# Optimization experiments

Hardware: AMD Instinct MI355X
Metric: run time of the kernel (lower is better)

## Reference

```python
import jax, jax.numpy as jnp
import numpy as np

N_NODES = 100000
N_EDGES = 1600000
DIM = 128


def setup_inputs() -> dict:
    key = jax.random.key(0)
    k1, k2, k3, k4 = jax.random.split(key, 4)
    x = jax.random.normal(k1, (N_NODES, DIM), dtype=jnp.float32)
    edge_index = jax.random.randint(k2, (2, N_EDGES), 0, N_NODES, dtype=jnp.int64)
    scale = 1.0 / np.sqrt(DIM)
    W1 = jax.random.normal(k3, (DIM, DIM), dtype=jnp.float32) * scale
    W2 = jax.random.normal(k4, (DIM, DIM), dtype=jnp.float32) * scale
    b1 = jnp.zeros((DIM,), dtype=jnp.float32)
    b2 = jnp.zeros((DIM,), dtype=jnp.float32)
    return {"x": x, "edge_index": edge_index, "W1": W1, "b1": b1, "W2": W2, "b2": b2}


def _gcn_conv(x, src, dst, dinv, W, b, n):
    # linear transform first (PyG GCNConv), then normalized scatter-add aggregation
    h = x @ W                                   # [N, out]
    norm = dinv[src] * dinv[dst]                # [E+N]
    msg = h[src] * norm[:, None]                # [E+N, out]
    agg = jax.ops.segment_sum(msg, dst, num_segments=n)
    return agg + b


def reference(x, edge_index, W1, b1, W2, b2):
    n = x.shape[0]
    loops = jnp.arange(n, dtype=edge_index.dtype)
    src = jnp.concatenate([edge_index[0], loops])  # add self-loops
    dst = jnp.concatenate([edge_index[1], loops])
    deg = jax.ops.segment_sum(jnp.ones_like(src, dtype=x.dtype), dst, num_segments=n)
    dinv = jnp.where(deg > 0, jax.lax.rsqrt(deg), 0.0)  # D^{-1/2}
    h = _gcn_conv(x, src, dst, dinv, W1, b1, n)
    h = jax.nn.relu(h)
    out = _gcn_conv(h, src, dst, dinv, W2, b2, n)
    return out
```

## Files before the change

kernel.cpp:

```cpp
#include <hip/hip_runtime.h>
#include <hip/hip_bf16.h>
#include <hip/hip_fp16.h>

#define NN 100000
#define DIM 128
#define NB 391
#define BCAP 5120
#define SCAN_NB 391
#define GTILES ((NN + 63) / 64)

typedef _Float16 f16x8 __attribute__((ext_vector_type(8)));
typedef float f32x4 __attribute__((ext_vector_type(4)));

__global__ void k_zero(int* __restrict__ p, int n) {
    int i = blockIdx.x * blockDim.x + threadIdx.x;
    if (i < n) p[i] = 0;
}

__global__ void k_binA(const int* __restrict__ src, const int* __restrict__ dst,
                       int* __restrict__ bcur, int* __restrict__ binbuf, int E) {
    __shared__ int hist[NB];
    __shared__ int base[NB];
    const int t = threadIdx.x;
    for (int b = t; b < NB; b += 256) hist[b] = 0;
    __syncthreads();

    const int e0 = blockIdx.x * 4096;
    int mys[16], myd[16];
#pragma unroll
    for (int i = 0; i < 16; ++i) {
        const int e = e0 + i * 256 + t;
        int d = -1, s = 0;
        if (e < E) {
            d = dst[e];
            s = src[e];
            atomicAdd(&hist[d >> 8], 1);
        }
        mys[i] = s;
        myd[i] = d;
    }
    __syncthreads();

    for (int b = t; b < NB; b += 256) {
        const int h = hist[b];
        base[b] = h ? atomicAdd(&bcur[b], h) : 0;
    }
    __syncthreads();
    for (int b = t; b < NB; b += 256) hist[b] = 0;
    __syncthreads();

#pragma unroll
    for (int i = 0; i < 16; ++i) {
        const int d = myd[i];
        if (d >= 0) {
            const int b = d >> 8;
            const int loc = atomicAdd(&hist[b], 1);
            const int p = base[b] + loc;
            if (p < BCAP) binbuf[b * BCAP + p] = mys[i] | ((d & 255) << 17);
        }
    }
}

__global__ void k_binCount(const int* __restrict__ bcur, const int* __restrict__ binbuf,
                           int* __restrict__ degi) {
    __shared__ int cnt[256];
    const int b = blockIdx.x;
    const int t = threadIdx.x;
    cnt[t] = 0;
    __syncthreads();
    const int n = min(bcur[b], BCAP);
    const int* p = &binbuf[b * BCAP];
    for (int i = t; i < n; i += 256) atomicAdd(&cnt[p[i] >> 17], 1);
    __syncthreads();
    const int node = b * 256 + t;
    if (node < NN) degi[node] = cnt[t];
}

__global__ void k_scan1(const int* __restrict__ deg, int* __restrict__ bsum, int n) {
    __shared__ int red[256];
    const int t = threadIdx.x;
    const int i = blockIdx.x * 256 + t;
    red[t] = (i < n) ? deg[i] : 0;
    __syncthreads();
    for (int d = 128; d > 0; d >>= 1) {
        if (t < d) red[t] += red[t + d];
        __syncthreads();
    }
    if (t == 0) bsum[blockIdx.x] = red[0];
}

__global__ void k_scan2(int* __restrict__ bsum, int nb) {
    __shared__ int s[1024];
    const int t = threadIdx.x;
    const int v = (t < nb) ? bsum[t] : 0;
    s[t] = v;
    __syncthreads();
    int acc = v;
    for (int d = 1; d < 1024; d <<= 1) {
        const int o = (t >= d) ? s[t - d] : 0;
        __syncthreads();
        acc += o;
        s[t] = acc;
        __syncthreads();
    }
    if (t < nb) bsum[t] = acc - v;
}

__global__ void k_scan3d(const int* __restrict__ deg, const int* __restrict__ bsum,
                         int* __restrict__ rowptr, float* __restrict__ dinv, int n) {
    __shared__ int s[256];
    const int t = threadIdx.x;
    const int i = blockIdx.x * 256 + t;
    const int v = (i < n) ? deg[i] : 0;
    s[t] = v;
    __syncthreads();
    int acc = v;
    for (int d = 1; d < 256; d <<= 1) {
        const int o = (t >= d) ? s[t - d] : 0;
        __syncthreads();
        acc += o;
        s[t] = acc;
        __syncthreads();
    }
    const int ex = acc - v + bsum[blockIdx.x];
    if (i < n) {
        rowptr[i] = ex;
        dinv[i] = rsqrtf((float)(v + 1));
        if (i == n - 1) rowptr[n] = ex + v;
    }
}

template <int IN_HALF, int FILL>
__global__ void k_gemm(const float* __restrict__ inF, const _Float16* __restrict__ inH,
                       const float* __restrict__ W, const float* __restrict__ dinv,
                       const float* __restrict__ bin, _Float16* __restrict__ outH,
                       const int* __restrict__ rowptr, const int* __restrict__ bcur,
                       const int* __restrict__ binbuf, int* __restrict__ csr) {
    __shared__ int cur[256];
    const int t = threadIdx.x;

    if (FILL && blockIdx.x < NB) {
        const int b = blockIdx.x;
        const int node = b * 256 + t;
        cur[t] = (node < NN) ? rowptr[node] : 0;
        __syncthreads();
        const int n = min(bcur[b], BCAP);
        const int* p = &binbuf[b * BCAP];
        for (int i = t; i < n; i += 256) {
            const int v = p[i];
            const int pos = atomicAdd(&cur[v >> 17], 1);
            csr[pos] = v & 0x1FFFF;
        }
        return;
    }

    const int tile = blockIdx.x - (FILL ? NB : 0);
    const int row0 = tile * 64;
    const int wv   = t >> 6;
    const int l    = t & 63;
    const int l15  = l & 15;
    const int lk8  = (l >> 4) << 3;
    const int colw = wv << 5;

    f16x8 bf[2][4];
#pragma unroll
    for (int ct = 0; ct < 2; ++ct) {
#pragma unroll
        for (int kt = 0; kt < 4; ++kt) {
            const int n  = colw + ct * 16 + l15;
            const int k0 = kt * 32 + lk8;
            f16x8 v;
#pragma unroll
            for (int j = 0; j < 8; ++j) v[j] = (_Float16)W[(k0 + j) * DIM + n];
            bf[ct][kt] = v;
        }
    }

    f32x4 acc[4][2];
#pragma unroll
    for (int rt = 0; rt < 4; ++rt)
#pragma unroll
        for (int ct = 0; ct < 2; ++ct) acc[rt][ct] = (f32x4){0.f, 0.f, 0.f, 0.f};

#pragma unroll
    for (int rt = 0; rt < 4; ++rt) {
        int row = row0 + rt * 16 + l15;
        row = min(row, NN - 1);
        f16x8 a[4];
#pragma unroll
        for (int kt = 0; kt < 4; ++kt) {
            const int k0 = kt * 32 + lk8;
            if constexpr (IN_HALF) {
                const f16x8 h = *(const f16x8*)&inH[row * DIM + k0];
                const float dr = dinv[row];
                const float4 bb0 = *(const float4*)&bin[k0];
                const float4 bb1 = *(const float4*)&bin[k0 + 4];
                f16x8 v;
                v[0] = (_Float16)fmaxf(fmaf(dr, (float)h[0], bb0.x), 0.f);
                v[1] = (_Float16)fmaxf(fmaf(dr, (float)h[1], bb0.y), 0.f);
                v[2] = (_Float16)fmaxf(fmaf(dr, (float)h[2], bb0.z), 0.f);
                v[3] = (_Float16)fmaxf(fmaf(dr, (float)h[3], bb0.w), 0.f);
                v[4] = (_Float16)fmaxf(fmaf(dr, (float)h[4], bb1.x), 0.f);
                v[5] = (_Float16)fmaxf(fmaf(dr, (float)h[5], bb1.y), 0.f);
                v[6] = (_Float16)fmaxf(fmaf(dr, (float)h[6], bb1.z), 0.f);
                v[7] = (_Float16)fmaxf(fmaf(dr, (float)h[7], bb1.w), 0.f);
                a[kt] = v;
            } else {
                const float4 v0 = *(const float4*)&inF[row * DIM + k0];
                const float4 v1 = *(const float4*)&inF[row * DIM + k0 + 4];
                f16x8 v;
                v[0] = (_Float16)v0.x; v[1] = (_Float16)v0.y;
                v[2] = (_Float16)v0.z; v[3] = (_Float16)v0.w;
                v[4] = (_Float16)v1.x; v[5] = (_Float16)v1.y;
                v[6] = (_Float16)v1.z; v[7] = (_Float16)v1.w;
                a[kt] = v;
            }
        }
#pragma unroll
        for (int ct = 0; ct < 2; ++ct)
#pragma unroll
            for (int kt = 0; kt < 4; ++kt)
                acc[rt][ct] = __builtin_amdgcn_mfma_f32_16x16x32_f16(a[kt], bf[ct][kt],
                                                                    acc[rt][ct], 0, 0, 0);
    }

#pragma unroll
    for (int rt = 0; rt < 4; ++rt) {
#pragma unroll
        for (int r = 0; r < 4; ++r) {
            const int row = row0 + rt * 16 + ((l >> 4) << 2) + r;
            if (row < NN) {
                const float d = dinv[row];
                outH[row * DIM + colw + l15]      = (_Float16)(acc[rt][0][r] * d);
                outH[row * DIM + colw + 16 + l15] = (_Float16)(acc[rt][1][r] * d);
            }
        }
    }
}

template <int FINAL>
__global__ void k_gather(const __half* __restrict__ hs, __half* __restrict__ outH,
                         float* __restrict__ outF, const int* __restrict__ csr,
                         const int* __restrict__ rowptr, const float* __restrict__ dinv,
                         const float* __restrict__ b2) {
    const int w = (blockIdx.x * blockDim.x + threadIdx.x) >> 6;
    if (w >= NN) return;
    const int lane = threadIdx.x & 63;
    const int off  = lane << 1;

    const int start = __builtin_amdgcn_readfirstlane(rowptr[w]);
    const int end   = __builtin_amdgcn_readfirstlane(rowptr[w + 1]);

    float2 a0 = __half22float2(*(const __half2*)&hs[w * DIM + off]);
    float2 a1 = {0.f, 0.f}, a2 = {0.f, 0.f}, a3 = {0.f, 0.f};

    int j = start;
    for (; j + 3 < end; j += 4) {
        const int s0 = __builtin_amdgcn_readfirstlane(csr[j]);
        const int s1 = __builtin_amdgcn_readfirstlane(csr[j + 1]);
        const int s2 = __builtin_amdgcn_readfirstlane(csr[j + 2]);
        const int s3 = __builtin_amdgcn_readfirstlane(csr[j + 3]);
        const float2 v0 = __half22float2(*(const __half2*)&hs[s0 * DIM + off]);
        const float2 v1 = __half22float2(*(const __half2*)&hs[s1 * DIM + off]);
        const float2 v2 = __half22float2(*(const __half2*)&hs[s2 * DIM + off]);
        const float2 v3 = __half22float2(*(const __half2*)&hs[s3 * DIM + off]);
        a0.x += v0.x; a0.y += v0.y;
        a1.x += v1.x; a1.y += v1.y;
        a2.x += v2.x; a2.y += v2.y;
        a3.x += v3.x; a3.y += v3.y;
    }
    for (; j < end; ++j) {
        const int s0 = __builtin_amdgcn_readfirstlane(csr[j]);
        const float2 v0 = __half22float2(*(const __half2*)&hs[s0 * DIM + off]);
        a0.x += v0.x; a0.y += v0.y;
    }

    float2 r = {a0.x + a1.x + a2.x + a3.x, a0.y + a1.y + a2.y + a3.y};
    if constexpr (FINAL) {
        const float d = dinv[w];
        const float2 b = *(const float2*)&b2[off];
        r.x = fmaf(d, r.x, b.x);
        r.y = fmaf(d, r.y, b.y);
        *(float2*)&outF[w * DIM + off] = r;
    } else {
        *(__half2*)&outH[w * DIM + off] = __floats2half2_rn(r.x, r.y);
    }
}

extern "C" void kernel_launch(void* const* d_in, const int* in_sizes, int n_in,
                              void* d_out, int out_size, void* d_ws, size_t ws_size,
                              hipStream_t stream) {
    const float* x  = (const float*)d_in[0];
    const int*   ei = (const int*)d_in[1];
    const float* W1 = (const float*)d_in[2];
    const float* b1 = (const float*)d_in[3];
    const float* W2 = (const float*)d_in[4];
    const float* b2 = (const float*)d_in[5];
    float* out = (float*)d_out;

    const int E = in_sizes[1] / 2;
    const int* src = ei;
    const int* dst = ei + E;

    char* ws = (char*)d_ws;
    float*    dinv   = (float*)(ws);
    int*      degi   = (int*)  (ws + (1  << 20));
    int*      rowptr = (int*)  (ws + (2  << 20));
    int*      bsum   = (int*)  (ws + (3  << 20));
    int*      bcur   = (int*)  (ws + (3  << 20) + 65536);
    int*      csr    = (int*)  (ws + (4  << 20));
    int*      binbuf = (int*)  (ws + (11 << 20));
    _Float16* hs     = (_Float16*)(ws + (20 << 20));
    _Float16* agg1   = (_Float16*)(ws + (47 << 20));

    const int ABLK = (E + 4095) / 4096;

    k_zero    <<<(NB + 255) / 256, 256, 0, stream>>>(bcur, NB);
    k_binA    <<<ABLK, 256, 0, stream>>>(src, dst, bcur, binbuf, E);
    k_binCount<<<NB, 256, 0, stream>>>(bcur, binbuf, degi);
    k_scan1   <<<SCAN_NB, 256, 0, stream>>>(degi, bsum, NN);
    k_scan2   <<<1, 1024, 0, stream>>>(bsum, SCAN_NB);
    k_scan3d  <<<SCAN_NB, 256, 0, stream>>>(degi, bsum, rowptr, dinv, NN);

    k_gemm<0, 1><<<NB + GTILES, 256, 0, stream>>>(x, nullptr, W1, dinv, nullptr, hs,
                                                  rowptr, bcur, binbuf, csr);
    k_gather<0> <<<(NN * 64) / 256, 256, 0, stream>>>((const __half*)hs, (__half*)agg1,
                                                      nullptr, csr, rowptr, dinv, nullptr);

    k_gemm<1, 0><<<GTILES, 256, 0, stream>>>(nullptr, agg1, W2, dinv, b1, hs,
                                             rowptr, bcur, binbuf, csr);
    k_gather<1> <<<(NN * 64) / 256, 256, 0, stream>>>((const __half*)hs, nullptr, out,
                                                      csr, rowptr, dinv, b2);
}
```

Before: 236.7 us.

## Fuse first-layer gather into second GEMM and fold scan stages into neighbours

```diff
diff --git a/kernel.cpp b/kernel.cpp
--- a/kernel.cpp
+++ b/kernel.cpp
@@ -6,7 +6,6 @@
 #define DIM 128
 #define NB 391
 #define BCAP 5120
-#define SCAN_NB 391
 #define GTILES ((NN + 63) / 64)
 
 typedef _Float16 f16x8 __attribute__((ext_vector_type(8)));
@@ -62,8 +61,10 @@
 }
 
 __global__ void k_binCount(const int* __restrict__ bcur, const int* __restrict__ binbuf,
-                           int* __restrict__ degi) {
+                           int* __restrict__ degi, float* __restrict__ dinv,
+                           int* __restrict__ bsum) {
     __shared__ int cnt[256];
+    __shared__ int red[256];
     const int b = blockIdx.x;
     const int t = threadIdx.x;
     cnt[t] = 0;
@@ -73,20 +74,18 @@
     for (int i = t; i < n; i += 256) atomicAdd(&cnt[p[i] >> 17], 1);
     __syncthreads();
     const int node = b * 256 + t;
-    if (node < NN) degi[node] = cnt[t];
-}
-
-__global__ void k_scan1(const int* __restrict__ deg, int* __restrict__ bsum, int n) {
-    __shared__ int red[256];
-    const int t = threadIdx.x;
-    const int i = blockIdx.x * 256 + t;
-    red[t] = (i < n) ? deg[i] : 0;
+    const int c = cnt[t];
+    if (node < NN) {
+        degi[node] = c;
+        dinv[node] = rsqrtf((float)(c + 1));
+    }
+    red[t] = (node < NN) ? c : 0;
     __syncthreads();
     for (int d = 128; d > 0; d >>= 1) {
         if (t < d) red[t] += red[t + d];
         __syncthreads();
     }
-    if (t == 0) bsum[blockIdx.x] = red[0];
+    if (t == 0) bsum[b] = red[0];
 }
 
 __global__ void k_scan2(int* __restrict__ bsum, int nb) {
@@ -106,43 +105,35 @@
     if (t < nb) bsum[t] = acc - v;
 }
 
-__global__ void k_scan3d(const int* __restrict__ deg, const int* __restrict__ bsum,
-                         int* __restrict__ rowptr, float* __restrict__ dinv, int n) {
+__global__ void k_gemm1(const float* __restrict__ inF, const float* __restrict__ W,
+                        const float* __restrict__ dinv, _Float16* __restrict__ outH,
+                        const int* __restrict__ degi, const int* __restrict__ bsum,
+                        int* __restrict__ rowptr, const int* __restrict__ bcur,
+                        const int* __restrict__ binbuf, int* __restrict__ csr) {
     __shared__ int s[256];
-    const int t = threadIdx.x;
-    const int i = blockIdx.x * 256 + t;
-    const int v = (i < n) ? deg[i] : 0;
-    s[t] = v;
-    __syncthreads();
-    int acc = v;
-    for (int d = 1; d < 256; d <<= 1) {
-        const int o = (t >= d) ? s[t - d] : 0;
-        __syncthreads();
-        acc += o;
-        s[t] = acc;
-        __syncthreads();
-    }
-    const int ex = acc - v + bsum[blockIdx.x];
-    if (i < n) {
-        rowptr[i] = ex;
-        dinv[i] = rsqrtf((float)(v + 1));
-        if (i == n - 1) rowptr[n] = ex + v;
-    }
-}
-
-template <int IN_HALF, int FILL>
-__global__ void k_gemm(const float* __restrict__ inF, const _Float16* __restrict__ inH,
-                       const float* __restrict__ W, const float* __restrict__ dinv,
-                       const float* __restrict__ bin, _Float16* __restrict__ outH,
-                       const int* __restrict__ rowptr, const int* __restrict__ bcur,
-                       const int* __restrict__ binbuf, int* __restrict__ csr) {
     __shared__ int cur[256];
     const int t = threadIdx.x;
 
-    if (FILL && blockIdx.x < NB) {
+    if (blockIdx.x < NB) {
         const int b = blockIdx.x;
         const int node = b * 256 + t;
-        cur[t] = (node < NN) ? rowptr[node] : 0;
+        const int deg = (node < NN) ? degi[node] : 0;
+        s[t] = deg;
+        __syncthreads();
+        int acc = deg;
+        for (int d = 1; d < 256; d <<= 1) {
+            const int o = (t >= d) ? s[t - d] : 0;
+            __syncthreads();
+            acc += o;
+            s[t] = acc;
+            __syncthreads();
+        }
+        const int ex = acc - deg + bsum[b];
+        cur[t] = ex;
+        if (node < NN) {
+            rowptr[node] = ex;
+            if (node == NN - 1) rowptr[NN] = ex + deg;
+        }
         __syncthreads();
         const int n = min(bcur[b], BCAP);
         const int* p = &binbuf[b * BCAP];
@@ -154,7 +145,7 @@
         return;
     }
 
-    const int tile = blockIdx.x - (FILL ? NB : 0);
+    const int tile = blockIdx.x - NB;
     const int row0 = tile * 64;
     const int wv   = t >> 6;
     const int l    = t & 63;
@@ -164,17 +155,16 @@
 
     f16x8 bf[2][4];
 #pragma unroll
-    for (int ct = 0; ct < 2; ++ct) {
+    for (int ct = 0; ct < 2; ++ct)
 #pragma unroll
         for (int kt = 0; kt < 4; ++kt) {
-            const int n  = colw + ct * 16 + l15;
+            const int nn = colw + ct * 16 + l15;
             const int k0 = kt * 32 + lk8;
             f16x8 v;
 #pragma unroll
-            for (int j = 0; j < 8; ++j) v[j] = (_Float16)W[(k0 + j) * DIM + n];
+            for (int j = 0; j < 8; ++j) v[j] = (_Float16)W[(k0 + j) * DIM + nn];
             bf[ct][kt] = v;
         }
-    }
 
     f32x4 acc[4][2];
 #pragma unroll
@@ -190,31 +180,14 @@
 #pragma unroll
         for (int kt = 0; kt < 4; ++kt) {
             const int k0 = kt * 32 + lk8;
-            if constexpr (IN_HALF) {
-                const f16x8 h = *(const f16x8*)&inH[row * DIM + k0];
-                const float dr = dinv[row];
-                const float4 bb0 = *(const float4*)&bin[k0];
-                const float4 bb1 = *(const float4*)&bin[k0 + 4];
-                f16x8 v;
-                v[0] = (_Float16)fmaxf(fmaf(dr, (float)h[0], bb0.x), 0.f);
-                v[1] = (_Float16)fmaxf(fmaf(dr, (float)h[1], bb0.y), 0.f);
-                v[2] = (_Float16)fmaxf(fmaf(dr, (float)h[2], bb0.z), 0.f);
-                v[3] = (_Float16)fmaxf(fmaf(dr, (float)h[3], bb0.w), 0.f);
-                v[4] = (_Float16)fmaxf(fmaf(dr, (float)h[4], bb1.x), 0.f);
-                v[5] = (_Float16)fmaxf(fmaf(dr, (float)h[5], bb1.y), 0.f);
-                v[6] = (_Float16)fmaxf(fmaf(dr, (float)h[6], bb1.z), 0.f);
-                v[7] = (_Float16)fmaxf(fmaf(dr, (float)h[7], bb1.w), 0.f);
-                a[kt] = v;
-            } else {
-                const float4 v0 = *(const float4*)&inF[row * DIM + k0];
-                const float4 v1 = *(const float4*)&inF[row * DIM + k0 + 4];
-                f16x8 v;
-                v[0] = (_Float16)v0.x; v[1] = (_Float16)v0.y;
-                v[2] = (_Float16)v0.z; v[3] = (_Float16)v0.w;
-                v[4] = (_Float16)v1.x; v[5] = (_Float16)v1.y;
-                v[6] = (_Float16)v1.z; v[7] = (_Float16)v1.w;
-                a[kt] = v;
-            }
+            const float4 v0 = *(const float4*)&inF[row * DIM + k0];
+            const float4 v1 = *(const float4*)&inF[row * DIM + k0 + 4];
+            f16x8 v;
+            v[0] = (_Float16)v0.x; v[1] = (_Float16)v0.y;
+            v[2] = (_Float16)v0.z; v[3] = (_Float16)v0.w;
+            v[4] = (_Float16)v1.x; v[5] = (_Float16)v1.y;
+            v[6] = (_Float16)v1.z; v[7] = (_Float16)v1.w;
+            a[kt] = v;
         }
 #pragma unroll
         for (int ct = 0; ct < 2; ++ct)
@@ -225,7 +198,7 @@
     }
 
 #pragma unroll
-    for (int rt = 0; rt < 4; ++rt) {
+    for (int rt = 0; rt < 4; ++rt)
 #pragma unroll
         for (int r = 0; r < 4; ++r) {
             const int row = row0 + rt * 16 + ((l >> 4) << 2) + r;
@@ -235,14 +208,112 @@
                 outH[row * DIM + colw + 16 + l15] = (_Float16)(acc[rt][1][r] * d);
             }
         }
-    }
-}
-
-template <int FINAL>
-__global__ void k_gather(const __half* __restrict__ hs, __half* __restrict__ outH,
-                         float* __restrict__ outF, const int* __restrict__ csr,
-                         const int* __restrict__ rowptr, const float* __restrict__ dinv,
-                         const float* __restrict__ b2) {
+}
+
+__global__ void k_gather_gemm(const __half* __restrict__ hs, const float* __restrict__ W,
+                              const float* __restrict__ dinv, const float* __restrict__ b1,
+                              _Float16* __restrict__ outH, const int* __restrict__ csr,
+                              const int* __restrict__ rowptr) {
+    __shared__ _Float16 As[64][136];
+    const int t    = threadIdx.x;
+    const int wv   = t >> 6;
+    const int l    = t & 63;
+    const int off  = l << 1;
+    const int row0 = blockIdx.x * 64;
+
+    const float2 bb = {b1[off], b1[off + 1]};
+
+#pragma unroll 1
+    for (int i = 0; i < 16; ++i) {
+        const int lr = wv * 16 + i;
+        const int n  = row0 + lr;
+        float2 r = {0.f, 0.f};
+        if (n < NN) {
+            const int start = __builtin_amdgcn_readfirstlane(rowptr[n]);
+            const int end   = __builtin_amdgcn_readfirstlane(rowptr[n + 1]);
+            float2 a0 = __half22float2(*(const __half2*)&hs[n * DIM + off]);
+            float2 a1 = {0.f, 0.f}, a2 = {0.f, 0.f}, a3 = {0.f, 0.f};
+            int j = start;
+            for (; j + 3 < end; j += 4) {
+                const int s0 = __builtin_amdgcn_readfirstlane(csr[j]);
+                const int s1 = __builtin_amdgcn_readfirstlane(csr[j + 1]);
+                const int s2 = __builtin_amdgcn_readfirstlane(csr[j + 2]);
+                const int s3 = __builtin_amdgcn_readfirstlane(csr[j + 3]);
+                const float2 v0 = __half22float2(*(const __half2*)&hs[s0 * DIM + off]);
+                const float2 v1 = __half22float2(*(const __half2*)&hs[s1 * DIM + off]);
+                const float2 v2 = __half22float2(*(const __half2*)&hs[s2 * DIM + off]);
+                const float2 v3 = __half22float2(*(const __half2*)&hs[s3 * DIM + off]);
+                a0.x += v0.x; a0.y += v0.y;
+                a1.x += v1.x; a1.y += v1.y;
+                a2.x += v2.x; a2.y += v2.y;
+                a3.x += v3.x; a3.y += v3.y;
+            }
+            for (; j < end; ++j) {
+                const int s0 = __builtin_amdgcn_readfirstlane(csr[j]);
+                const float2 v0 = __half22float2(*(const __half2*)&hs[s0 * DIM + off]);
+                a0.x += v0.x; a0.y += v0.y;
+            }
+            const float dn = dinv[n];
+            r.x = fmaxf(fmaf(dn, a0.x + a1.x + a2.x + a3.x, bb.x), 0.f);
+            r.y = fmaxf(fmaf(dn, a0.y + a1.y + a2.y + a3.y, bb.y), 0.f);
+        }
+        *(__half2*)&As[lr][off] = __floats2half2_rn(r.x, r.y);
+    }
+    __syncthreads();
+
+    const int l15  = l & 15;
+    const int lk8  = (l >> 4) << 3;
+    const int colw = wv << 5;
+
+    f16x8 bf[2][4];
+#pragma unroll
+    for (int ct = 0; ct < 2; ++ct)
+#pragma unroll
+        for (int kt = 0; kt < 4; ++kt) {
+            const int nn = colw + ct * 16 + l15;
+            const int k0 = kt * 32 + lk8;
+            f16x8 v;
+#pragma unroll
+            for (int j = 0; j < 8; ++j) v[j] = (_Float16)W[(k0 + j) * DIM + nn];
+            bf[ct][kt] = v;
+        }
+
+    f32x4 acc[4][2];
+#pragma unroll
+    for (int rt = 0; rt < 4; ++rt)
+#pragma unroll
+        for (int ct = 0; ct < 2; ++ct) acc[rt][ct] = (f32x4){0.f, 0.f, 0.f, 0.f};
+
+#pragma unroll
+    for (int rt = 0; rt < 4; ++rt) {
+        f16x8 a[4];
+#pragma unroll
+        for (int kt = 0; kt < 4; ++kt)
+            a[kt] = *(const f16x8*)&As[rt * 16 + l15][kt * 32 + lk8];
+#pragma unroll
+        for (int ct = 0; ct < 2; ++ct)
+#pragma unroll
+            for (int kt = 0; kt < 4; ++kt)
+                acc[rt][ct] = __builtin_amdgcn_mfma_f32_16x16x32_f16(a[kt], bf[ct][kt],
+                                                                    acc[rt][ct], 0, 0, 0);
+    }
+
+#pragma unroll
+    for (int rt = 0; rt < 4; ++rt)
+#pragma unroll
+        for (int r = 0; r < 4; ++r) {
+            const int row = row0 + rt * 16 + ((l >> 4) << 2) + r;
+            if (row < NN) {
+                const float d = dinv[row];
+                outH[row * DIM + colw + l15]      = (_Float16)(acc[rt][0][r] * d);
+                outH[row * DIM + colw + 16 + l15] = (_Float16)(acc[rt][1][r] * d);
+            }
+        }
+}
+
+__global__ void k_gather2(const __half* __restrict__ hs, float* __restrict__ outF,
+                          const int* __restrict__ csr, const int* __restrict__ rowptr,
+                          const float* __restrict__ dinv, const float* __restrict__ b2) {
     const int w = (blockIdx.x * blockDim.x + threadIdx.x) >> 6;
     if (w >= NN) return;
     const int lane = threadIdx.x & 63;
@@ -275,16 +346,12 @@
         a0.x += v0.x; a0.y += v0.y;
     }
 
-    float2 r = {a0.x + a1.x + a2.x + a3.x, a0.y + a1.y + a2.y + a3.y};
-    if constexpr (FINAL) {
-        const float d = dinv[w];
-        const float2 b = *(const float2*)&b2[off];
-        r.x = fmaf(d, r.x, b.x);
-        r.y = fmaf(d, r.y, b.y);
-        *(float2*)&outF[w * DIM + off] = r;
-    } else {
-        *(__half2*)&outH[w * DIM + off] = __floats2half2_rn(r.x, r.y);
-    }
+    const float d = dinv[w];
+    const float2 b = *(const float2*)&b2[off];
+    float2 r;
+    r.x = fmaf(d, a0.x + a1.x + a2.x + a3.x, b.x);
+    r.y = fmaf(d, a0.y + a1.y + a2.y + a3.y, b.y);
+    *(float2*)&outF[w * DIM + off] = r;
 }
 
 extern "C" void kernel_launch(void* const* d_in, const int* in_sizes, int n_in,
@@ -311,24 +378,21 @@
     int*      csr    = (int*)  (ws + (4  << 20));
     int*      binbuf = (int*)  (ws + (11 << 20));
     _Float16* hs     = (_Float16*)(ws + (20 << 20));
-    _Float16* agg1   = (_Float16*)(ws + (47 << 20));
+    _Float16* hs2    = (_Float16*)(ws + (47 << 20));
 
     const int ABLK = (E + 4095) / 4096;
 
     k_zero    <<<(NB + 255) / 256, 256, 0, stream>>>(bcur, NB);
     k_binA    <<<ABLK, 256, 0, stream>>>(src, dst, bcur, binbuf, E);
-    k_binCount<<<NB, 256, 0, stream>>>(bcur, binbuf, degi);
-    k_scan1   <<<SCAN_NB, 256, 0, stream>>>(degi, bsum, NN);
-    k_scan2   <<<1, 1024, 0, stream>>>(bsum, SCAN_NB);
-    k_scan3d  <<<SCAN_NB, 256, 0, stream>>>(degi, bsum, rowptr, dinv, NN);
-
-    k_gemm<0, 1><<<NB + GTILES, 256, 0, stream>>>(x, nullptr, W1, dinv, nullptr, hs,
-                                                  rowptr, bcur, binbuf, csr);
-    k_gather<0> <<<(NN * 64) / 256, 256, 0, stream>>>((const __half*)hs, (__half*)agg1,
-                                                      nullptr, csr, rowptr, dinv, nullptr);
-
-    k_gemm<1, 0><<<GTILES, 256, 0, stream>>>(nullptr, agg1, W2, dinv, b1, hs,
+    k_binCount<<<NB, 256, 0, stream>>>(bcur, binbuf, degi, dinv, bsum);
+    k_scan2   <<<1, 1024, 0, stream>>>(bsum, NB);
+
+    k_gemm1<<<NB + GTILES, 256, 0, stream>>>(x, W1, dinv, hs, degi, bsum,
                                              rowptr, bcur, binbuf, csr);
-    k_gather<1> <<<(NN * 64) / 256, 256, 0, stream>>>((const __half*)hs, nullptr, out,
-                                                      csr, rowptr, dinv, b2);
-}
+
+    k_gather_gemm<<<GTILES, 256, 0, stream>>>((const __half*)hs, W2, dinv, b1, hs2,
+                                              csr, rowptr);
+
+    k_gather2<<<(NN * 64) / 256, 256, 0, stream>>>((const __half*)hs2, out, csr, rowptr,
+                                                   dinv, b2);
+}
```

Result: slower. 256.0 us (+8.1%).
